# Performance work log

Hardware: AMD Instinct MI355X
Metric: run time of the kernel (lower is better)

## Reference

```python
import jax, jax.numpy as jnp
import numpy as np

N_NODES = 100000
N_EDGES = 1600000
IN_DIM, HID_DIM, OUT_DIM = 512, 128, 64


def gcn_layer(x, rows, cols, vals, W, b):
    # support = x @ W; out[i] = sum_{e: rows[e]==i} vals[e] * support[cols[e]] + b
    support = x @ W                      # [N, d_out]
    msgs = vals[:, None] * support[cols]  # [E, d_out] gather
    agg = jax.ops.segment_sum(msgs, rows, num_segments=N_NODES)  # scatter-add
    return agg + b


def setup_inputs() -> dict:
    key = jax.random.key(0)
    ks = jax.random.split(key, 8)
    x = jax.random.normal(ks[0], (N_NODES, IN_DIM), dtype=jnp.float32)
    edge_rows = jax.random.randint(ks[1], (N_EDGES,), 0, N_NODES, dtype=jnp.int32)
    edge_cols = jax.random.randint(ks[2], (N_EDGES,), 0, N_NODES, dtype=jnp.int32)
    edge_vals = jax.random.uniform(ks[3], (N_EDGES,), dtype=jnp.float32)
    W0 = jax.random.normal(ks[4], (IN_DIM, HID_DIM), dtype=jnp.float32) / np.sqrt(IN_DIM)
    b0 = jnp.zeros((HID_DIM,), dtype=jnp.float32)
    W1 = jax.random.normal(ks[5], (HID_DIM, OUT_DIM), dtype=jnp.float32) / np.sqrt(HID_DIM)
    b1 = jnp.zeros((OUT_DIM,), dtype=jnp.float32)
    return {"x": x, "edge_rows": edge_rows, "edge_cols": edge_cols,
            "edge_vals": edge_vals, "W0": W0, "b0": b0, "W1": W1, "b1": b1}


def reference(x, edge_rows, edge_cols, edge_vals, W0, b0, W1, b1):
    h = gcn_layer(x, edge_rows, edge_cols, edge_vals, W0, b0)  # GCN0
    h = jax.nn.relu(h)                                          # activation0
    # dropout: identity in eval mode
    out = gcn_layer(h, edge_rows, edge_cols, edge_vals, W1, b1)  # GCN1
    return out
```

## Files before the change

### kernel.cpp

```cpp
#include <hip/hip_runtime.h>

#define N_NODES 100000
#define N_EDGES 1600000
#define NBUCK   ((N_NODES + 127) / 128)
#define BCAP    4096

typedef __attribute__((ext_vector_type(8))) short bf16x8;
typedef __attribute__((ext_vector_type(4))) float f32x4;

__device__ __forceinline__ unsigned short f2bf(float f) {
    unsigned int u = __builtin_bit_cast(unsigned int, f);
    u = (u + 0x7FFFu + ((u >> 16) & 1u)) >> 16;
    return (unsigned short)u;
}
__device__ __forceinline__ float bfu2f(unsigned short u) {
    return __builtin_bit_cast(float, (unsigned int)u << 16);
}
__device__ __forceinline__ uint2 packbf4(float4 v) {
    uint2 p;
    p.x = (unsigned int)f2bf(v.x) | ((unsigned int)f2bf(v.y) << 16);
    p.y = (unsigned int)f2bf(v.z) | ((unsigned int)f2bf(v.w) << 16);
    return p;
}

__device__ __forceinline__ void block_barrier() {
    asm volatile("s_waitcnt lgkmcnt(0)" ::: "memory");
    __builtin_amdgcn_sched_barrier(0);
    __builtin_amdgcn_s_barrier();
    __builtin_amdgcn_sched_barrier(0);
}

__global__ __launch_bounds__(256) void prep_kernel(const float* __restrict__ W0,
                                                   const float* __restrict__ W1,
                                                   unsigned short* __restrict__ W0t,
                                                   unsigned short* __restrict__ W1t,
                                                   int* __restrict__ bcursor) {
    const int i = blockIdx.x * 256 + threadIdx.x;
    if (i < 512 * 128) {
        const int k = i / 128, c = i % 128;
        W0t[c * 512 + k] = f2bf(W0[i]);
    }
    const int j = i - 512 * 128;
    if (j >= 0 && j < 128 * 64) {
        const int k = j / 64, c = j % 64;
        W1t[c * 128 + k] = f2bf(W1[j]);
    }
    const int z = i - (512 * 128 + 128 * 64);
    if (z >= 0 && z < NBUCK) bcursor[z] = z * BCAP;
}

__global__ __launch_bounds__(256) void gemm1_kernel(const float* __restrict__ A,
                                                    const unsigned short* __restrict__ Wt,
                                                    unsigned short* __restrict__ C, int N) {
    constexpr int K   = 512;
    constexpr int M   = 128;
    constexpr int LDT = 40;

    __shared__ __align__(16) unsigned short As[2][64 * LDT];
    __shared__ __align__(16) unsigned short Bs[2][M * LDT];

    const int tid  = threadIdx.x;
    const int lane = tid & 63;
    const int wid  = tid >> 6;
    const int wm   = wid >> 1;
    const int wn   = wid & 1;
    const int brow = blockIdx.x * 64;

    const int ar0 = tid >> 3, akq = tid & 7;
    const int ar1 = ar0 + 32;
    const bool v0 = (brow + ar0) < N;
    const bool v1 = (brow + ar1) < N;
    const float* ap0 = A + (size_t)(brow + ar0) * K + akq * 4;
    const float* ap1 = A + (size_t)(brow + ar1) * K + akq * 4;
    const int br0 = tid >> 2, bkq = tid & 3;
    const unsigned short* bp0 = Wt + (size_t)br0 * K + bkq * 8;
    const unsigned short* bp1 = Wt + (size_t)(br0 + 64) * K + bkq * 8;

    float4 A0a, A0b, A1a, A1b, A2a, A2b, A3a, A3b;
    uint4  B0a, B0b, B1a, B1b, B2a, B2b, B3a, B3b;

#define ISSUE(s, t) do {                                                          \
        const int ko = (t) * 32;                                                  \
        A##s##a = v0 ? *reinterpret_cast<const float4*>(ap0 + ko)                 \
                     : make_float4(0.f, 0.f, 0.f, 0.f);                           \
        A##s##b = v1 ? *reinterpret_cast<const float4*>(ap1 + ko)                 \
                     : make_float4(0.f, 0.f, 0.f, 0.f);                           \
        B##s##a = *reinterpret_cast<const uint4*>(bp0 + ko);                      \
        B##s##b = *reinterpret_cast<const uint4*>(bp1 + ko);                      \
    } while (0)

#define WLDS(s, buf) do {                                                         \
        *reinterpret_cast<uint2*>(&As[buf][ar0 * LDT + akq * 4]) = packbf4(A##s##a); \
        *reinterpret_cast<uint2*>(&As[buf][ar1 * LDT + akq * 4]) = packbf4(A##s##b); \
        *reinterpret_cast<uint4*>(&Bs[buf][br0 * LDT + bkq * 8]) = B##s##a;          \
        *reinterpret_cast<uint4*>(&Bs[buf][(br0 + 64) * LDT + bkq * 8]) = B##s##b;   \
    } while (0)

    f32x4 acc[2][4];
#pragma unroll
    for (int m = 0; m < 2; ++m)
#pragma unroll
        for (int n = 0; n < 4; ++n) acc[m][n] = (f32x4){0.f, 0.f, 0.f, 0.f};

    const int afo = (wm * 32 + (lane & 15)) * LDT + (lane >> 4) * 8;
    const int bfo = (wn * 64 + (lane & 15)) * LDT + (lane >> 4) * 8;

    auto step = [&](int buf) {
        bf16x8 af[2], bfr[4];
#pragma unroll
        for (int m = 0; m < 2; ++m)
            af[m] = *reinterpret_cast<const bf16x8*>(&As[buf][afo + m * 16 * LDT]);
#pragma unroll
        for (int n = 0; n < 4; ++n)
            bfr[n] = *reinterpret_cast<const bf16x8*>(&Bs[buf][bfo + n * 16 * LDT]);
#pragma unroll
        for (int m = 0; m < 2; ++m)
#pragma unroll
            for (int n = 0; n < 4; ++n)
                acc[m][n] = __builtin_amdgcn_mfma_f32_16x16x32_bf16(af[m], bfr[n], acc[m][n], 0, 0, 0);
    };

    ISSUE(0, 0); ISSUE(1, 1); ISSUE(2, 2); ISSUE(3, 3);
    WLDS(0, 0);
    block_barrier();

#pragma unroll
    for (int i = 0; i < 4; ++i) {
        const int t = 4 * i;
        if (t + 4 < 16) ISSUE(0, t + 4);
        step(0);
        WLDS(1, 1);
        block_barrier();
        if (t + 5 < 16) ISSUE(1, t + 5);
        step(1);
        WLDS(2, 0);
        block_barrier();
        if (t + 6 < 16) ISSUE(2, t + 6);
        step(0);
        WLDS(3, 1);
        block_barrier();
        if (t + 7 < 16) ISSUE(3, t + 7);
        step(1);
        if (t + 4 < 16) WLDS(0, 0);
        block_barrier();
    }
#undef ISSUE
#undef WLDS

    const int rb = brow + wm * 32 + ((lane >> 4) * 4);
    const int cb = wn * 64 + (lane & 15);
#pragma unroll
    for (int m = 0; m < 2; ++m)
#pragma unroll
        for (int n = 0; n < 4; ++n)
#pragma unroll
            for (int j = 0; j < 4; ++j) {
                const int r = rb + m * 16 + j;
                if (r < N) C[(size_t)r * M + cb + n * 16] = f2bf(acc[m][n][j]);
            }
}

__global__ __launch_bounds__(256) void gemm2_kernel(const unsigned short* __restrict__ Hb,
                                                    const unsigned short* __restrict__ Wt,
                                                    unsigned short* __restrict__ C) {
    const int gw = (blockIdx.x * 256 + threadIdx.x) >> 6;
    if (gw >= N_NODES / 16) return;
    const int lane = threadIdx.x & 63;
    const int rlo = lane & 15, khi = lane >> 4;
    const int rb = gw * 16;

    const unsigned short* wp = Wt + (size_t)rlo * 128 + khi * 8;
    bf16x8 b[4][4];
#pragma unroll
    for (int n = 0; n < 4; ++n)
#pragma unroll
        for (int t = 0; t < 4; ++t)
            b[n][t] = *reinterpret_cast<const bf16x8*>(wp + (size_t)n * 16 * 128 + t * 32);

    f32x4 acc[4];
#pragma unroll
    for (int n = 0; n < 4; ++n) acc[n] = (f32x4){0.f, 0.f, 0.f, 0.f};

    const unsigned short* hp = Hb + (size_t)(rb + rlo) * 128 + khi * 8;
#pragma unroll
    for (int t = 0; t < 4; ++t) {
        const bf16x8 af = *reinterpret_cast<const bf16x8*>(hp + t * 32);
#pragma unroll
        for (int n = 0; n < 4; ++n)
            acc[n] = __builtin_amdgcn_mfma_f32_16x16x32_bf16(af, b[n][t], acc[n], 0, 0, 0);
    }

#pragma unroll
    for (int n = 0; n < 4; ++n)
#pragma unroll
        for (int j = 0; j < 4; ++j)
            C[(size_t)(rb + khi * 4 + j) * 64 + n * 16 + rlo] = f2bf(acc[n][j]);
}

#define SCAT_CH 4096
__global__ __launch_bounds__(256) void scatter_bucket_kernel(const int* __restrict__ rows,
                                                             const int* __restrict__ cols,
                                                             const float* __restrict__ vals,
                                                             int* __restrict__ bcursor,
                                                             int2* __restrict__ tmp) {
    __shared__ int hist[NBUCK];
    const int tid = threadIdx.x;
    const int e0  = blockIdx.x * SCAT_CH;

    int   er[16];
    int   ec[16];
    float ev[16];
#pragma unroll
    for (int i = 0; i < 16; ++i) {
        const int e = e0 + i * 256 + tid;
        const bool ok = e < N_EDGES;
        er[i] = ok ? rows[e] : -1;
        ec[i] = ok ? cols[e] : 0;
        ev[i] = ok ? vals[e] : 0.f;
    }

    for (int b = tid; b < NBUCK; b += 256) hist[b] = 0;
    __syncthreads();

#pragma unroll
    for (int i = 0; i < 16; ++i)
        if (er[i] >= 0) atomicAdd(&hist[er[i] >> 7], 1);
    __syncthreads();

    for (int b = tid; b < NBUCK; b += 256) {
        const int hcnt = hist[b];
        hist[b] = (hcnt > 0) ? atomicAdd(&bcursor[b], hcnt) : 0;
    }
    __syncthreads();

#pragma unroll
    for (int i = 0; i < 16; ++i) {
        if (er[i] >= 0) {
            const int pos = atomicAdd(&hist[er[i] >> 7], 1);
            tmp[pos] = make_int2(ec[i] | ((er[i] & 127) << 17), __float_as_int(ev[i]));
        }
    }
}

template<int DIM, bool RELU_BF16_OUT>
__global__ __launch_bounds__(512) void spmm_bucket_kernel(const int* __restrict__ bcursor,
                                                          const int2* __restrict__ tmp,
                                                          const unsigned short* __restrict__ sup,
                                                          const float* __restrict__ bias,
                                                          void* __restrict__ aggv) {
    constexpr int GL = DIM / 8;
    constexpr int NG = 64 / GL;

    __shared__ int2 eds[BCAP];
    __shared__ int  cnt_sh[128];
    __shared__ int  startsh[128];
    __shared__ int  cur[128];

    const int b    = blockIdx.x;
    const int tid  = threadIdx.x;
    const int base = b * BCAP;
    const int cnt  = bcursor[b] - base;

    int2 w[8];
#pragma unroll
    for (int i = 0; i < 8; ++i) {
        const int j = i * 512 + tid;
        w[i] = (j < cnt) ? tmp[base + j] : make_int2(-1, 0);
    }
    if (tid < 128) cnt_sh[tid] = 0;
    __syncthreads();
#pragma unroll
    for (int i = 0; i < 8; ++i)
        if (w[i].x >= 0) atomicAdd(&cnt_sh[((unsigned int)w[i].x) >> 17], 1);
    __syncthreads();

    if (tid == 0) {
        int a = 0;
        for (int i = 0; i < 128; ++i) { startsh[i] = a; a += cnt_sh[i]; }
    }
    __syncthreads();
    if (tid < 128) cur[tid] = startsh[tid];
    __syncthreads();

#pragma unroll
    for (int i = 0; i < 8; ++i) {
        if (w[i].x >= 0) {
            const int rl  = ((unsigned int)w[i].x) >> 17;
            const int pos = atomicAdd(&cur[rl], 1);
            eds[pos] = make_int2(w[i].x & 0x1FFFF, w[i].y);
        }
    }
    __syncthreads();

    const int lane = tid & 63;
    const int wid  = tid >> 6;
    const int grp  = lane / GL;
    const int sub  = lane % GL;

    for (int r8 = 0; r8 < 16; ++r8) {
        const int rl  = wid * 16 + r8;
        const int row = (b << 7) + rl;
        const int start = startsh[rl];
        const int end   = start + cnt_sh[rl];

        float a[8] = {0.f, 0.f, 0.f, 0.f, 0.f, 0.f, 0.f, 0.f};

        int j = start + grp;
        while (j + NG < end) {
            const int2 e0 = eds[j];
            const int2 e1 = eds[j + NG];
            const bf16x8 s0 = *reinterpret_cast<const bf16x8*>(sup + (size_t)e0.x * DIM + sub * 8);
            const bf16x8 s1 = *reinterpret_cast<const bf16x8*>(sup + (size_t)e1.x * DIM + sub * 8);
            const float v0 = __int_as_float(e0.y);
            const float v1 = __int_as_float(e1.y);
#pragma unroll
            for (int d = 0; d < 8; ++d) a[d] = fmaf(v0, bfu2f((unsigned short)s0[d]), a[d]);
#pragma unroll
            for (int d = 0; d < 8; ++d) a[d] = fmaf(v1, bfu2f((unsigned short)s1[d]), a[d]);
            j += 2 * NG;
        }
        for (; j < end; j += NG) {
            const int2 e = eds[j];
            const bf16x8 s = *reinterpret_cast<const bf16x8*>(sup + (size_t)e.x * DIM + sub * 8);
            const float v = __int_as_float(e.y);
#pragma unroll
            for (int d = 0; d < 8; ++d) a[d] = fmaf(v, bfu2f((unsigned short)s[d]), a[d]);
        }

#pragma unroll
        for (int d = 0; d < 8; ++d) {
            if (GL == 8) a[d] += __shfl_xor(a[d], 8);
            a[d] += __shfl_xor(a[d], 16);
            a[d] += __shfl_xor(a[d], 32);
        }

        if (lane < GL && row < N_NODES) {
            const float4 b0 = *reinterpret_cast<const float4*>(bias + sub * 8);
            const float4 b1 = *reinterpret_cast<const float4*>(bias + sub * 8 + 4);
            float o[8];
            o[0] = a[0] + b0.x; o[1] = a[1] + b0.y; o[2] = a[2] + b0.z; o[3] = a[3] + b0.w;
            o[4] = a[4] + b1.x; o[5] = a[5] + b1.y; o[6] = a[6] + b1.z; o[7] = a[7] + b1.w;
            if (RELU_BF16_OUT) {
                unsigned short* hb = (unsigned short*)aggv;
                bf16x8 r;
#pragma unroll
                for (int d = 0; d < 8; ++d) r[d] = (short)f2bf(fmaxf(o[d], 0.f));
                *reinterpret_cast<bf16x8*>(hb + (size_t)row * DIM + sub * 8) = r;
            } else {
                float* og = (float*)aggv;
                float* dst = og + (size_t)row * DIM + sub * 8;
                *reinterpret_cast<float4*>(dst)     = make_float4(o[0], o[1], o[2], o[3]);
                *reinterpret_cast<float4*>(dst + 4) = make_float4(o[4], o[5], o[6], o[7]);
            }
        }
    }
}

extern "C" void kernel_launch(void* const* d_in, const int* in_sizes, int n_in,
                              void* d_out, int out_size, void* d_ws, size_t ws_size,
                              hipStream_t stream) {
    const float* x    = (const float*)d_in[0];
    const int*   rows = (const int*)d_in[1];
    const int*   cols = (const int*)d_in[2];
    const float* vals = (const float*)d_in[3];
    const float* W0   = (const float*)d_in[4];
    const float* b0   = (const float*)d_in[5];
    const float* W1   = (const float*)d_in[6];
    const float* b1   = (const float*)d_in[7];
    float*       out  = (float*)d_out;

    char* p = (char*)d_ws;
    unsigned short* sup0 = (unsigned short*)p;  p += (size_t)N_NODES * 128 * 2;
    unsigned short* h    = (unsigned short*)p;  p += (size_t)N_NODES * 128 * 2;
    unsigned short* sup1 = (unsigned short*)p;  p += (size_t)N_NODES * 64 * 2;
    unsigned short* W0t  = (unsigned short*)p;  p += (size_t)512 * 128 * 2;
    unsigned short* W1t  = (unsigned short*)p;  p += (size_t)128 * 64 * 2;
    int*   bcursor  = (int*)p;                  p += (size_t)((NBUCK + 3) / 4) * 16;
    int2*  tmp      = (int2*)p;                 p += (size_t)NBUCK * BCAP * 8;

    const int prep_blocks = (512 * 128 + 128 * 64 + NBUCK + 255) / 256;
    const int scat_blocks = (N_EDGES + SCAT_CH - 1) / SCAT_CH;
    const int gemm_blocks = (N_NODES + 63) / 64;
    const int gem2_blocks = (N_NODES / 16 + 3) / 4;

    prep_kernel<<<prep_blocks, 256, 0, stream>>>(W0, W1, W0t, W1t, bcursor);

    scatter_bucket_kernel<<<scat_blocks, 256, 0, stream>>>(rows, cols, vals, bcursor, tmp);

    gemm1_kernel<<<gemm_blocks, 256, 0, stream>>>(x, W0t, sup0, N_NODES);
    spmm_bucket_kernel<128, true><<<NBUCK, 512, 0, stream>>>(bcursor, tmp, sup0, b0, h);

    gemm2_kernel<<<gem2_blocks, 256, 0, stream>>>(h, W1t, sup1);
    spmm_bucket_kernel<64, false><<<NBUCK, 512, 0, stream>>>(bcursor, tmp, sup1, b1, out);
}
```

Measured before the change: 218.7 us.

## Fuse second-layer GEMM into first SpMM epilogue via wave-level MFMA

The first SpMM now applies bias and ReLU, gathers each wave's 16 aggregated rows into MFMA A-fragments through cross-lane shuffles, and multiplies by W1 directly to produce sup1. This removes the intermediate h buffer write and read and one kernel launch. The cost is extra shuffles per row and W1 fragment loads in every SpMM wave, which may raise register pressure.

After: 220.3 us. About the same (+0.7%).

```diff
diff --git a/kernel.cpp b/kernel.cpp
--- a/kernel.cpp
+++ b/kernel.cpp
@@ -160,43 +160,6 @@
             }
 }
 
-__global__ __launch_bounds__(256) void gemm2_kernel(const unsigned short* __restrict__ Hb,
-                                                    const unsigned short* __restrict__ Wt,
-                                                    unsigned short* __restrict__ C) {
-    const int gw = (blockIdx.x * 256 + threadIdx.x) >> 6;
-    if (gw >= N_NODES / 16) return;
-    const int lane = threadIdx.x & 63;
-    const int rlo = lane & 15, khi = lane >> 4;
-    const int rb = gw * 16;
-
-    const unsigned short* wp = Wt + (size_t)rlo * 128 + khi * 8;
-    bf16x8 b[4][4];
-#pragma unroll
-    for (int n = 0; n < 4; ++n)
-#pragma unroll
-        for (int t = 0; t < 4; ++t)
-            b[n][t] = *reinterpret_cast<const bf16x8*>(wp + (size_t)n * 16 * 128 + t * 32);
-
-    f32x4 acc[4];
-#pragma unroll
-    for (int n = 0; n < 4; ++n) acc[n] = (f32x4){0.f, 0.f, 0.f, 0.f};
-
-    const unsigned short* hp = Hb + (size_t)(rb + rlo) * 128 + khi * 8;
-#pragma unroll
-    for (int t = 0; t < 4; ++t) {
-        const bf16x8 af = *reinterpret_cast<const bf16x8*>(hp + t * 32);
-#pragma unroll
-        for (int n = 0; n < 4; ++n)
-            acc[n] = __builtin_amdgcn_mfma_f32_16x16x32_bf16(af, b[n][t], acc[n], 0, 0, 0);
-    }
-
-#pragma unroll
-    for (int n = 0; n < 4; ++n)
-#pragma unroll
-        for (int j = 0; j < 4; ++j)
-            C[(size_t)(rb + khi * 4 + j) * 64 + n * 16 + rlo] = f2bf(acc[n][j]);
-}
-
 #define SCAT_CH 4096
 __global__ __launch_bounds__(256) void scatter_bucket_kernel(const int* __restrict__ rows,
                                                              const int* __restrict__ cols,
@@ -242,14 +205,15 @@
     }
 }
 
-template<int DIM, bool RELU_BF16_OUT>
-__global__ __launch_bounds__(512) void spmm_bucket_kernel(const int* __restrict__ bcursor,
-                                                          const int2* __restrict__ tmp,
-                                                          const unsigned short* __restrict__ sup,
-                                                          const float* __restrict__ bias,
-                                                          void* __restrict__ aggv) {
-    constexpr int GL = DIM / 8;
-    constexpr int NG = 64 / GL;
+__global__ __launch_bounds__(512) void spmm_gcn0_kernel(const int* __restrict__ bcursor,
+                                                        const int2* __restrict__ tmp,
+                                                        const unsigned short* __restrict__ sup,
+                                                        const float* __restrict__ bias,
+                                                        const unsigned short* __restrict__ W1t,
+                                                        unsigned short* __restrict__ sup1) {
+    constexpr int DIM = 128;
+    constexpr int GL  = 16;
+    constexpr int NG  = 4;
 
     __shared__ int2 eds[BCAP];
     __shared__ int  cnt_sh[128];
@@ -294,12 +258,18 @@
 
     const int lane = tid & 63;
     const int wid  = tid >> 6;
-    const int grp  = lane / GL;
-    const int sub  = lane % GL;
+    const int khi  = lane >> 4;
+    const int rlo  = lane & 15;
+    const int grp  = khi;
+    const int sub  = rlo;
+
+    const float4 bb0 = *reinterpret_cast<const float4*>(bias + sub * 8);
+    const float4 bb1 = *reinterpret_cast<const float4*>(bias + sub * 8 + 4);
+
+    bf16x8 afr[4];
 
     for (int r8 = 0; r8 < 16; ++r8) {
-        const int rl  = wid * 16 + r8;
-        const int row = (b << 7) + rl;
+        const int rl    = wid * 16 + r8;
         const int start = startsh[rl];
         const int end   = start + cnt_sh[rl];
 
@@ -329,7 +299,148 @@
 
 #pragma unroll
         for (int d = 0; d < 8; ++d) {
-            if (GL == 8) a[d] += __shfl_xor(a[d], 8);
+            a[d] += __shfl_xor(a[d], 16);
+            a[d] += __shfl_xor(a[d], 32);
+        }
+
+        bf16x8 pk;
+        pk[0] = (short)f2bf(fmaxf(a[0] + bb0.x, 0.f));
+        pk[1] = (short)f2bf(fmaxf(a[1] + bb0.y, 0.f));
+        pk[2] = (short)f2bf(fmaxf(a[2] + bb0.z, 0.f));
+        pk[3] = (short)f2bf(fmaxf(a[3] + bb0.w, 0.f));
+        pk[4] = (short)f2bf(fmaxf(a[4] + bb1.x, 0.f));
+        pk[5] = (short)f2bf(fmaxf(a[5] + bb1.y, 0.f));
+        pk[6] = (short)f2bf(fmaxf(a[6] + bb1.z, 0.f));
+        pk[7] = (short)f2bf(fmaxf(a[7] + bb1.w, 0.f));
+        const uint4 pu = __builtin_bit_cast(uint4, pk);
+
+#pragma unroll
+        for (int t = 0; t < 4; ++t) {
+            const int src = t * 4 + khi;
+            uint4 g;
+            g.x = (unsigned int)__shfl((int)pu.x, src);
+            g.y = (unsigned int)__shfl((int)pu.y, src);
+            g.z = (unsigned int)__shfl((int)pu.z, src);
+            g.w = (unsigned int)__shfl((int)pu.w, src);
+            if (rlo == r8) afr[t] = __builtin_bit_cast(bf16x8, g);
+        }
+    }
+
+    const unsigned short* wp = W1t + (size_t)rlo * 128 + khi * 8;
+    bf16x8 bf_[4][4];
+#pragma unroll
+    for (int n = 0; n < 4; ++n)
+#pragma unroll
+        for (int t = 0; t < 4; ++t)
+            bf_[n][t] = *reinterpret_cast<const bf16x8*>(wp + (size_t)n * 16 * 128 + t * 32);
+
+    f32x4 acc2[4];
+#pragma unroll
+    for (int n = 0; n < 4; ++n) acc2[n] = (f32x4){0.f, 0.f, 0.f, 0.f};
+#pragma unroll
+    for (int t = 0; t < 4; ++t)
+#pragma unroll
+        for (int n = 0; n < 4; ++n)
+            acc2[n] = __builtin_amdgcn_mfma_f32_16x16x32_bf16(afr[t], bf_[n][t], acc2[n], 0, 0, 0);
+
+    const int rb2 = (b << 7) + wid * 16 + khi * 4;
+#pragma unroll
+    for (int n = 0; n < 4; ++n)
+#pragma unroll
+        for (int j = 0; j < 4; ++j) {
+            const int r = rb2 + j;
+            if (r < N_NODES) sup1[(size_t)r * 64 + n * 16 + rlo] = f2bf(acc2[n][j]);
+        }
+}
+
+__global__ __launch_bounds__(512) void spmm_bucket64_kernel(const int* __restrict__ bcursor,
+                                                            const int2* __restrict__ tmp,
+                                                            const unsigned short* __restrict__ sup,
+                                                            const float* __restrict__ bias,
+                                                            float* __restrict__ outg) {
+    constexpr int DIM = 64;
+    constexpr int GL  = 8;
+    constexpr int NG  = 8;
+
+    __shared__ int2 eds[BCAP];
+    __shared__ int  cnt_sh[128];
+    __shared__ int  startsh[128];
+    __shared__ int  cur[128];
+
+    const int b    = blockIdx.x;
+    const int tid  = threadIdx.x;
+    const int base = b * BCAP;
+    const int cnt  = bcursor[b] - base;
+
+    int2 w[8];
+#pragma unroll
+    for (int i = 0; i < 8; ++i) {
+        const int j = i * 512 + tid;
+        w[i] = (j < cnt) ? tmp[base + j] : make_int2(-1, 0);
+    }
+    if (tid < 128) cnt_sh[tid] = 0;
+    __syncthreads();
+#pragma unroll
+    for (int i = 0; i < 8; ++i)
+        if (w[i].x >= 0) atomicAdd(&cnt_sh[((unsigned int)w[i].x) >> 17], 1);
+    __syncthreads();
+
+    if (tid == 0) {
+        int a = 0;
+        for (int i = 0; i < 128; ++i) { startsh[i] = a; a += cnt_sh[i]; }
+    }
+    __syncthreads();
+    if (tid < 128) cur[tid] = startsh[tid];
+    __syncthreads();
+
+#pragma unroll
+    for (int i = 0; i < 8; ++i) {
+        if (w[i].x >= 0) {
+            const int rl  = ((unsigned int)w[i].x) >> 17;
+            const int pos = atomicAdd(&cur[rl], 1);
+            eds[pos] = make_int2(w[i].x & 0x1FFFF, w[i].y);
+        }
+    }
+    __syncthreads();
+
+    const int lane = tid & 63;
+    const int wid  = tid >> 6;
+    const int grp  = lane / GL;
+    const int sub  = lane % GL;
+
+    for (int r8 = 0; r8 < 16; ++r8) {
+        const int rl  = wid * 16 + r8;
+        const int row = (b << 7) + rl;
+        const int start = startsh[rl];
+        const int end   = start + cnt_sh[rl];
+
+        float a[8] = {0.f, 0.f, 0.f, 0.f, 0.f, 0.f, 0.f, 0.f};
+
+        int j = start + grp;
+        while (j + NG < end) {
+            const int2 e0 = eds[j];
+            const int2 e1 = eds[j + NG];
+            const bf16x8 s0 = *reinterpret_cast<const bf16x8*>(sup + (size_t)e0.x * DIM + sub * 8);
+            const bf16x8 s1 = *reinterpret_cast<const bf16x8*>(sup + (size_t)e1.x * DIM + sub * 8);
+            const float v0 = __int_as_float(e0.y);
+            const float v1 = __int_as_float(e1.y);
+#pragma unroll
+            for (int d = 0; d < 8; ++d) a[d] = fmaf(v0, bfu2f((unsigned short)s0[d]), a[d]);
+#pragma unroll
+            for (int d = 0; d < 8; ++d) a[d] = fmaf(v1, bfu2f((unsigned short)s1[d]), a[d]);
+            j += 2 * NG;
+        }
+        for (; j < end; j += NG) {
+            const int2 e = eds[j];
+            const bf16x8 s = *reinterpret_cast<const bf16x8*>(sup + (size_t)e.x * DIM + sub * 8);
+            const float v = __int_as_float(e.y);
+#pragma unroll
+            for (int d = 0; d < 8; ++d) a[d] = fmaf(v, bfu2f((unsigned short)s[d]), a[d]);
+        }
+
+#pragma unroll
+        for (int d = 0; d < 8; ++d) {
+            a[d] += __shfl_xor(a[d], 8);
             a[d] += __shfl_xor(a[d], 16);
             a[d] += __shfl_xor(a[d], 32);
         }
@@ -337,21 +448,9 @@
         if (lane < GL && row < N_NODES) {
             const float4 b0 = *reinterpret_cast<const float4*>(bias + sub * 8);
             const float4 b1 = *reinterpret_cast<const float4*>(bias + sub * 8 + 4);
-            float o[8];
-            o[0] = a[0] + b0.x; o[1] = a[1] + b0.y; o[2] = a[2] + b0.z; o[3] = a[3] + b0.w;
-            o[4] = a[4] + b1.x; o[5] = a[5] + b1.y; o[6] = a[6] + b1.z; o[7] = a[7] + b1.w;
-            if (RELU_BF16_OUT) {
-                unsigned short* hb = (unsigned short*)aggv;
-                bf16x8 r;
-#pragma unroll
-                for (int d = 0; d < 8; ++d) r[d] = (short)f2bf(fmaxf(o[d], 0.f));
-                *reinterpret_cast<bf16x8*>(hb + (size_t)row * DIM + sub * 8) = r;
-            } else {
-                float* og = (float*)aggv;
-                float* dst = og + (size_t)row * DIM + sub * 8;
-                *reinterpret_cast<float4*>(dst)     = make_float4(o[0], o[1], o[2], o[3]);
-                *reinterpret_cast<float4*>(dst + 4) = make_float4(o[4], o[5], o[6], o[7]);
-            }
+            float* dst = outg + (size_t)row * DIM + sub * 8;
+            *reinterpret_cast<float4*>(dst)     = make_float4(a[0] + b0.x, a[1] + b0.y, a[2] + b0.z, a[3] + b0.w);
+            *reinterpret_cast<float4*>(dst + 4) = make_float4(a[4] + b1.x, a[5] + b1.y, a[6] + b1.z, a[7] + b1.w);
         }
     }
 }
@@ -371,7 +470,6 @@
 
     char* p = (char*)d_ws;
     unsigned short* sup0 = (unsigned short*)p;  p += (size_t)N_NODES * 128 * 2;
-    unsigned short* h    = (unsigned short*)p;  p += (size_t)N_NODES * 128 * 2;
     unsigned short* sup1 = (unsigned short*)p;  p += (size_t)N_NODES * 64 * 2;
     unsigned short* W0t  = (unsigned short*)p;  p += (size_t)512 * 128 * 2;
     unsigned short* W1t  = (unsigned short*)p;  p += (size_t)128 * 64 * 2;
@@ -381,15 +479,14 @@
     const int prep_blocks = (512 * 128 + 128 * 64 + NBUCK + 255) / 256;
     const int scat_blocks = (N_EDGES + SCAT_CH - 1) / SCAT_CH;
     const int gemm_blocks = (N_NODES + 63) / 64;
-    const int gem2_blocks = (N_NODES / 16 + 3) / 4;
 
     prep_kernel<<<prep_blocks, 256, 0, stream>>>(W0, W1, W0t, W1t, bcursor);
 
     scatter_bucket_kernel<<<scat_blocks, 256, 0, stream>>>(rows, cols, vals, bcursor, tmp);
 
     gemm1_kernel<<<gemm_blocks, 256, 0, stream>>>(x, W0t, sup0, N_NODES);
-    spmm_bucket_kernel<128, true><<<NBUCK, 512, 0, stream>>>(bcursor, tmp, sup0, b0, h);
-
-    gemm2_kernel<<<gem2_blocks, 256, 0, stream>>>(h, W1t, sup1);
-    spmm_bucket_kernel<64, false><<<NBUCK, 512, 0, stream>>>(bcursor, tmp, sup1, b1, out);
-}
+
+    spmm_gcn0_kernel<<<NBUCK, 512, 0, stream>>>(bcursor, tmp, sup0, b0, W1t, sup1);
+
+    spmm_bucket64_kernel<<<NBUCK, 512, 0, stream>>>(bcursor, tmp, sup1, b1, out);
+}
```
